# Performance work log

Measured on AMD Instinct MI355X. Metric: run time of the kernel, lower is better.

## Reference

```python
import jax, jax.numpy as jnp
import numpy as np

N_NODES = 100000
N_EDGES = 1600000
D_IN = 128
D_HID = 128
D_OUT = 128


def setup_inputs() -> dict:
    key = jax.random.key(0)
    ks = jax.random.split(key, 6)
    node_features = jax.random.normal(ks[0], (N_NODES, D_IN), dtype=jnp.float32)
    edge_index = jax.random.randint(ks[1], (2, N_EDGES), 0, N_NODES, dtype=jnp.int32)
    s1 = 1.0 / np.sqrt(D_IN)
    s2 = 1.0 / np.sqrt(D_HID)
    W1 = jax.random.normal(ks[2], (D_IN, D_HID), dtype=jnp.float32) * s1
    W2 = jax.random.normal(ks[3], (D_HID, D_HID), dtype=jnp.float32) * s2
    W3 = jax.random.normal(ks[4], (D_HID, D_OUT), dtype=jnp.float32) * s2
    b1 = jnp.zeros((D_HID,), dtype=jnp.float32)
    b2 = jnp.zeros((D_HID,), dtype=jnp.float32)
    b3 = jnp.zeros((D_OUT,), dtype=jnp.float32)
    return {"node_features": node_features, "edge_index": edge_index,
            "W1": W1, "b1": b1, "W2": W2, "b2": b2, "W3": W3, "b3": b3}


def _aggregate(x, src, dst, n_nodes):
    # mean over incoming neighbors (by dst), residual add; degree clamped to >=1
    msg = jax.ops.segment_sum(x[src], dst, num_segments=n_nodes)  # [N, D]
    deg = jax.ops.segment_sum(jnp.ones_like(dst, dtype=x.dtype), dst,
                              num_segments=n_nodes)
    deg = jnp.maximum(deg, 1.0)[:, None]
    return x + msg / deg


def reference(node_features, edge_index, W1, b1, W2, b2, W3, b3):
    n_nodes = node_features.shape[0]
    src, dst = edge_index[0], edge_index[1]
    x = _aggregate(node_features, src, dst, n_nodes)
    x = jax.nn.relu(x @ W1 + b1)
    x = _aggregate(x, src, dst, n_nodes)
    x = jax.nn.relu(x @ W2 + b2)
    x = x.mean(axis=0)  # graph readout -> [D_HID]
    return x @ W3 + b3  # [D_OUT]
```

## Files before the change

### kernel.cpp

```cpp
#include <hip/hip_runtime.h>

#define D 128
#define SLOTS 64
#define NB 391
#define NBANK 4
#define SUBCAP 1536
#define BINCAP (NBANK * SUBCAP)
#define BATCH 2048
#define EPB 8
#define CNTSTRIDE 16
#define WPITCH 136

typedef __attribute__((ext_vector_type(8))) short short8;
typedef __attribute__((ext_vector_type(4))) float float4v;

__device__ inline unsigned short f2bf(float f) {
    union { float f; unsigned u; } a; a.f = f;
    unsigned u = a.u;
    return (unsigned short)((u + 0x7fffu + ((u >> 16) & 1u)) >> 16);
}
__device__ inline unsigned packbf(float a, float b) {
    return (unsigned)f2bf(a) | ((unsigned)f2bf(b) << 16);
}
__device__ inline unsigned pack4fp8(float a, float b, float c, float d) {
    int t = __builtin_amdgcn_cvt_pk_fp8_f32(a, b, 0, false);
    t = __builtin_amdgcn_cvt_pk_fp8_f32(c, d, t, true);
    return (unsigned)t;
}
__device__ inline unsigned char pack1fp8(float a) {
    int t = __builtin_amdgcn_cvt_pk_fp8_f32(a, 0.f, 0, false);
    return (unsigned char)(t & 0xff);
}
__device__ inline void acc8fp8(float* acc, uint2 w) {
    auto f0 = __builtin_amdgcn_cvt_pk_f32_fp8(w.x, false);
    auto f1 = __builtin_amdgcn_cvt_pk_f32_fp8(w.x, true);
    auto f2 = __builtin_amdgcn_cvt_pk_f32_fp8(w.y, false);
    auto f3 = __builtin_amdgcn_cvt_pk_f32_fp8(w.y, true);
    acc[0] += f0[0]; acc[1] += f0[1]; acc[2] += f1[0]; acc[3] += f1[1];
    acc[4] += f2[0]; acc[5] += f2[1]; acc[6] += f3[0]; acc[7] += f3[1];
}


__global__ __launch_bounds__(256) void k_head(const int* __restrict__ src,
                                              const int* __restrict__ dst, int nE,
                                              int* __restrict__ gcnt, int* __restrict__ bins,
                                              const float* __restrict__ x,
                                              unsigned char* __restrict__ y8,
                                              unsigned char* __restrict__ h8dummy,
                                              float* __restrict__ colsum,
                                              int n16, int nBatches) {
    __shared__ int hist[512];
    __shared__ int excl[512];
    __shared__ int base[NB];
    __shared__ int stage[BATCH];
    __shared__ int gofs[BATCH];
    __shared__ int waveSum[4];
    int tid = threadIdx.x;

    if (blockIdx.x >= nBatches) {
        int cb = blockIdx.x - nBatches;
        if (cb == 0) {
            if (tid < 128) colsum[tid] = 0.f;
            else if (tid < 136)
                reinterpret_cast<uint4*>(y8)[(size_t)n16 + (tid - 128)] = make_uint4(0, 0, 0, 0);
            else if (tid < 144)
                reinterpret_cast<uint4*>(h8dummy)[tid - 136] = make_uint4(0, 0, 0, 0);
        }
        int i = cb * 256 + tid;
        if (i < n16) {
            const float4* xin = reinterpret_cast<const float4*>(x) + (size_t)i * 4;
            float4 v0 = xin[0], v1 = xin[1], v2 = xin[2], v3 = xin[3];
            uint4 o;
            o.x = pack4fp8(v0.x, v0.y, v0.z, v0.w);
            o.y = pack4fp8(v1.x, v1.y, v1.z, v1.w);
            o.z = pack4fp8(v2.x, v2.y, v2.z, v2.w);
            o.w = pack4fp8(v3.x, v3.y, v3.z, v3.w);
            reinterpret_cast<uint4*>(y8)[i] = o;
        }
        return;
    }

    int start = blockIdx.x * BATCH;
    int cntB = nE - start; if (cntB > BATCH) cntB = BATCH;
    if (cntB <= 0) return;
    int bank = blockIdx.x & (NBANK - 1);

    hist[tid] = 0; hist[tid + 256] = 0;
    __syncthreads();

    int b[EPB], r[EPB], v[EPB];
    #pragma unroll
    for (int i = 0; i < EPB; ++i) {
        int e = start + i * 256 + tid;
        if (e < nE) {
            int d = dst[e];
            b[i] = d >> 8;
            v[i] = (src[e] << 8) | (d & 255);
            r[i] = atomicAdd(&hist[b[i]], 1);
        } else b[i] = -1;
    }
    __syncthreads();

    int e0 = tid * 2, e1 = e0 + 1;
    int h0 = hist[e0], h1v = hist[e1];
    int s = h0 + h1v;
    int lane = tid & 63, w = tid >> 6;
    int sum = s;
    #pragma unroll
    for (int off2 = 1; off2 < 64; off2 <<= 1) {
        int tmp = __shfl_up(sum, off2, 64);
        if (lane >= off2) sum += tmp;
    }
    if (lane == 63) waveSum[w] = sum;
    __syncthreads();
    int wbase = 0;
    if (w > 0) wbase += waveSum[0];
    if (w > 1) wbase += waveSum[1];
    if (w > 2) wbase += waveSum[2];
    int exclPair = wbase + sum - s;
    excl[e0] = exclPair;
    excl[e1] = exclPair + h0;
    if (tid < NB)
        base[tid] = atomicAdd(&gcnt[(tid * NBANK + bank) * CNTSTRIDE], hist[tid]);
    if (tid + 256 < NB)
        base[tid + 256] = atomicAdd(&gcnt[((tid + 256) * NBANK + bank) * CNTSTRIDE], hist[tid + 256]);
    __syncthreads();

    #pragma unroll
    for (int i = 0; i < EPB; ++i) {
        if (b[i] >= 0) {
            int p = excl[b[i]] + r[i];
            int o = base[b[i]] + r[i];
            stage[p] = v[i];
            gofs[p] = (o < SUBCAP) ? (b[i] * BINCAP + bank * SUBCAP + o) : -1;
        }
    }
    __syncthreads();

    #pragma unroll
    for (int i = 0; i < EPB; ++i) {
        int p = i * 256 + tid;
        if (p < cntB) {
            int g = gofs[p];
            if (g >= 0) bins[g] = stage[p];
        }
    }
}


__global__ __launch_bounds__(256) void k_scatter2(const int* __restrict__ gcnt,
                                                  const int* __restrict__ bins,
                                                  int* __restrict__ slots,
                                                  int* __restrict__ deg, int n, int nAll) {
    __shared__ int slotsL[128 * SLOTS];
    __shared__ int cntL[128];
    __shared__ int cnt4s[128];
    int tid = threadIdx.x;
    int bin = blockIdx.x >> 1;
    int half = blockIdx.x & 1;
    if (tid < 128) cntL[tid] = 0;
    __syncthreads();

    #pragma unroll
    for (int k = 0; k < NBANK; ++k) {
        int c = gcnt[(bin * NBANK + k) * CNTSTRIDE]; if (c > SUBCAP) c = SUBCAP;
        const int* eb = bins + (size_t)bin * BINCAP + k * SUBCAP;
        for (int i = tid; i < c; i += 256) {
            int vv = eb[i];
            int dl = vv & 255;
            if ((dl >> 7) == half) {
                int p = atomicAdd(&cntL[dl & 127], 1);
                if (p < SLOTS) slotsL[(dl & 127) * SLOTS + p] = vv >> 8;
            }
        }
    }
    __syncthreads();

    int node0 = bin * 256 + half * 128;
    int remNodes = n - node0;
    if (remNodes > 128) remNodes = 128;
    if (remNodes < 0) remNodes = 0;

    if (tid < remNodes) {
        int dg = cntL[tid]; if (dg > SLOTS) dg = SLOTS;
        int dgr = (dg + 3) & ~3;
        for (int p = dg; p < dgr; ++p) slotsL[tid * SLOTS + p] = nAll;
        deg[node0 + tid] = dg;
        cnt4s[tid] = dgr;
    }
    __syncthreads();

    uint4* gout = reinterpret_cast<uint4*>(slots + (size_t)node0 * SLOTS);
    const uint4* lin = reinterpret_cast<const uint4*>(slotsL);
    int nv = remNodes * (SLOTS / 4);
    for (int i = tid; i < nv; i += 256) {
        int nd = i >> 4, vec = i & 15;
        if ((vec << 2) < cnt4s[nd]) gout[i] = lin[i];
    }
}


__global__ void k_agg(const unsigned char* __restrict__ Xin8,
                      unsigned short* __restrict__ Xout,
                      const int* __restrict__ deg, const int* __restrict__ slots, int n) {
    int t = blockIdx.x * 256 + threadIdx.x;
    int node = t >> 4;
    int lane = t & 15;
    if (node >= n) return;
    int dg = deg[node];
    int cnt4 = (dg + 3) & ~3;
    float acc[8] = {0.f, 0.f, 0.f, 0.f, 0.f, 0.f, 0.f, 0.f};
    const int* sl = slots + (size_t)node * SLOTS;
    for (int j = 0; j < cnt4; j += 4) {
        int4 s4 = *reinterpret_cast<const int4*>(sl + j);
        uint2 w0 = *reinterpret_cast<const uint2*>(Xin8 + (size_t)s4.x * D + lane * 8);
        uint2 w1 = *reinterpret_cast<const uint2*>(Xin8 + (size_t)s4.y * D + lane * 8);
        uint2 w2 = *reinterpret_cast<const uint2*>(Xin8 + (size_t)s4.z * D + lane * 8);
        uint2 w3 = *reinterpret_cast<const uint2*>(Xin8 + (size_t)s4.w * D + lane * 8);
        acc8fp8(acc, w0); acc8fp8(acc, w1); acc8fp8(acc, w2); acc8fp8(acc, w3);
    }
    float inv = 1.0f / (float)(dg > 0 ? dg : 1);
    uint2 s8 = *reinterpret_cast<const uint2*>(Xin8 + (size_t)node * D + lane * 8);
    float self[8] = {0.f, 0.f, 0.f, 0.f, 0.f, 0.f, 0.f, 0.f};
    acc8fp8(self, s8);
    float o[8];
    #pragma unroll
    for (int k = 0; k < 8; ++k) o[k] = self[k] + acc[k] * inv;
    uint4 ov;
    ov.x = packbf(o[0], o[1]); ov.y = packbf(o[2], o[3]);
    ov.z = packbf(o[4], o[5]); ov.w = packbf(o[6], o[7]);
    reinterpret_cast<uint4*>(Xout + (size_t)node * D)[lane] = ov;
}


__global__ __launch_bounds__(256) void k_gemm(const unsigned short* __restrict__ X,
                                              const float* __restrict__ W,
                                              const float* __restrict__ bias,
                                              unsigned char* __restrict__ Y8,
                                              float* __restrict__ colsum,
                                              int n, int mode) {
    __shared__ unsigned short Wt[128 * WPITCH];
    __shared__ float cs[128];
    int tid = threadIdx.x;
    int wave = tid >> 6, L = tid & 63;
    int m16 = L & 15, g = L >> 4;

    #pragma unroll
    for (int i = 0; i < 8; ++i) {
        int p = i * 256 + tid;
        int col = p & 127, kg = p >> 7;
        unsigned pk[4];
        #pragma unroll
        for (int h = 0; h < 4; ++h) {
            float w0 = W[(kg * 8 + 2 * h + 0) * 128 + col];
            float w1 = W[(kg * 8 + 2 * h + 1) * 128 + col];
            pk[h] = packbf(w0, w1);
        }
        *reinterpret_cast<uint4*>(&Wt[col * WPITCH + kg * 8]) =
            make_uint4(pk[0], pk[1], pk[2], pk[3]);
    }
    if (mode && tid < 128) cs[tid] = 0.f;
    __syncthreads();

    int row0 = blockIdx.x * 128 + wave * 32;
    float4v zero4 = {0.f, 0.f, 0.f, 0.f};
    float4v acc[2][8];
    #pragma unroll
    for (int rt = 0; rt < 2; ++rt)
        #pragma unroll
        for (int ct = 0; ct < 8; ++ct) acc[rt][ct] = zero4;

    #pragma unroll
    for (int q = 0; q < 4; ++q) {
        int k0 = q * 32;
        short8 a[2];
        #pragma unroll
        for (int rt = 0; rt < 2; ++rt) {
            int row = row0 + rt * 16 + m16;
            short8 af = {0, 0, 0, 0, 0, 0, 0, 0};
            if (row < n)
                af = *reinterpret_cast<const short8*>(X + (size_t)row * D + k0 + g * 8);
            a[rt] = af;
        }
        #pragma unroll
        for (int ct = 0; ct < 8; ++ct) {
            short8 b = *reinterpret_cast<const short8*>(&Wt[(ct * 16 + m16) * WPITCH + k0 + g * 8]);
            acc[0][ct] = __builtin_amdgcn_mfma_f32_16x16x32_bf16(a[0], b, acc[0][ct], 0, 0, 0);
            acc[1][ct] = __builtin_amdgcn_mfma_f32_16x16x32_bf16(a[1], b, acc[1][ct], 0, 0, 0);
        }
    }

    float bj[8];
    #pragma unroll
    for (int ct = 0; ct < 8; ++ct) bj[ct] = bias[ct * 16 + m16];

    if (mode == 0) {
        #pragma unroll
        for (int rt = 0; rt < 2; ++rt)
            #pragma unroll
            for (int i = 0; i < 4; ++i) {
                int row = row0 + rt * 16 + g * 4 + i;
                if (row < n) {
                    #pragma unroll
                    for (int ct = 0; ct < 8; ++ct) {
                        float v = fmaxf(acc[rt][ct][i] + bj[ct], 0.f);
                        Y8[(size_t)row * D + ct * 16 + m16] = pack1fp8(v);
                    }
                }
            }
    } else {
        float csv[8] = {0.f, 0.f, 0.f, 0.f, 0.f, 0.f, 0.f, 0.f};
        #pragma unroll
        for (int rt = 0; rt < 2; ++rt)
            #pragma unroll
            for (int i = 0; i < 4; ++i) {
                int row = row0 + rt * 16 + g * 4 + i;
                if (row < n) {
                    #pragma unroll
                    for (int ct = 0; ct < 8; ++ct)
                        csv[ct] += fmaxf(acc[rt][ct][i] + bj[ct], 0.f);
                }
            }
        #pragma unroll
        for (int ct = 0; ct < 8; ++ct) atomicAdd(&cs[ct * 16 + m16], csv[ct]);
        __syncthreads();
        if (tid < 128) atomicAdd(&colsum[tid], cs[tid]);
    }
}


__global__ void k_final(const float* __restrict__ colsum, const float* __restrict__ W3,
                        const float* __restrict__ b3, float* __restrict__ out, float invN) {
    int j = threadIdx.x;
    float acc = b3[j];
    #pragma unroll 8
    for (int k = 0; k < D; ++k)
        acc += colsum[k] * invN * W3[k * D + j];
    out[j] = acc;
}


extern "C" void kernel_launch(void* const* d_in, const int* in_sizes, int n_in,
                              void* d_out, int out_size, void* d_ws, size_t ws_size,
                              hipStream_t stream) {
    const float* nf = (const float*)d_in[0];
    const int*   ei = (const int*)d_in[1];
    const float* W1 = (const float*)d_in[2];
    const float* b1 = (const float*)d_in[3];
    const float* W2 = (const float*)d_in[4];
    const float* b2 = (const float*)d_in[5];
    const float* W3 = (const float*)d_in[6];
    const float* b3 = (const float*)d_in[7];
    float* out = (float*)d_out;

    int n  = in_sizes[0] / D;
    int nE = in_sizes[1] / 2;
    const int* src = ei;
    const int* dst = ei + nE;

    int nBins = (n + 255) / 256;
    int nBatches = (nE + BATCH - 1) / BATCH;
    int n16 = n * (D / 16);

    char* ws = (char*)d_ws;
    size_t off = 0;
    auto alloc = [&](size_t bytes) -> void* {
        off = (off + 255) & ~(size_t)255;
        void* p = ws + off;
        off += bytes;
        return p;
    };
    int* gcnt  = (int*)alloc((size_t)nBins * NBANK * CNTSTRIDE * 4);
    int* bins  = (int*)alloc((size_t)nBins * BINCAP * 4);
    int* slots = (int*)alloc((size_t)nBins * 256 * SLOTS * 4);
    int* deg   = (int*)alloc((size_t)n * 4);
    unsigned char*  x8  = (unsigned char*) alloc((size_t)(n + 1) * D);
    unsigned short* t16 = (unsigned short*)alloc((size_t)n * D * 2);
    unsigned char*  h8  = (unsigned char*) alloc((size_t)(n + 1) * D);
    float* colsum = (float*)alloc(128 * 4);

    hipMemsetAsync(gcnt, 0, (size_t)nBins * NBANK * CNTSTRIDE * 4, stream);

    int gC = (n16 + 255) / 256;
    int gA = (n * 16 + 255) / 256;
    int gG = (n + 127) / 128;

    k_head<<<nBatches + gC, 256, 0, stream>>>(src, dst, nE, gcnt, bins,
                                              nf, x8, h8 + (size_t)n * D,
                                              colsum, n16, nBatches);
    k_scatter2<<<nBins * 2, 256, 0, stream>>>(gcnt, bins, slots, deg, n, n);

    k_agg<<<gA, 256, 0, stream>>>(x8, t16, deg, slots, n);
    k_gemm<<<gG, 256, 0, stream>>>(t16, W1, b1, h8, (float*)nullptr, n, 0);
    k_agg<<<gA, 256, 0, stream>>>(h8, t16, deg, slots, n);
    k_gemm<<<gG, 256, 0, stream>>>(t16, W2, b2, (unsigned char*)nullptr, colsum, n, 1);
    k_final<<<1, 128, 0, stream>>>(colsum, W3, b3, out, 1.0f / (float)n);
}
```

Measured before the change: 257.1 us.

## Fuse final readout into last GEMM block, widen gather unroll, more count banks

```diff
diff --git a/kernel.cpp b/kernel.cpp
--- a/kernel.cpp
+++ b/kernel.cpp
@@ -3,8 +3,8 @@
 #define D 128
 #define SLOTS 64
 #define NB 391
-#define NBANK 4
-#define SUBCAP 1536
+#define NBANK 8
+#define SUBCAP 768
 #define BINCAP (NBANK * SUBCAP)
 #define BATCH 2048
 #define EPB 8
@@ -154,7 +154,7 @@
                                                   int* __restrict__ deg, int n, int nAll) {
     __shared__ int slotsL[128 * SLOTS];
     __shared__ int cntL[128];
-    __shared__ int cnt4s[128];
+    __shared__ int cnt8s[128];
     int tid = threadIdx.x;
     int bin = blockIdx.x >> 1;
     int half = blockIdx.x & 1;
@@ -183,10 +183,10 @@
 
     if (tid < remNodes) {
         int dg = cntL[tid]; if (dg > SLOTS) dg = SLOTS;
-        int dgr = (dg + 3) & ~3;
+        int dgr = (dg + 7) & ~7;
         for (int p = dg; p < dgr; ++p) slotsL[tid * SLOTS + p] = nAll;
         deg[node0 + tid] = dg;
-        cnt4s[tid] = dgr;
+        cnt8s[tid] = dgr;
     }
     __syncthreads();
 
@@ -195,7 +195,7 @@
     int nv = remNodes * (SLOTS / 4);
     for (int i = tid; i < nv; i += 256) {
         int nd = i >> 4, vec = i & 15;
-        if ((vec << 2) < cnt4s[nd]) gout[i] = lin[i];
+        if ((vec << 2) < cnt8s[nd]) gout[i] = lin[i];
     }
 }
 
@@ -208,16 +208,22 @@
     int lane = t & 15;
     if (node >= n) return;
     int dg = deg[node];
-    int cnt4 = (dg + 3) & ~3;
+    int cnt8 = (dg + 7) & ~7;
     float acc[8] = {0.f, 0.f, 0.f, 0.f, 0.f, 0.f, 0.f, 0.f};
     const int* sl = slots + (size_t)node * SLOTS;
-    for (int j = 0; j < cnt4; j += 4) {
-        int4 s4 = *reinterpret_cast<const int4*>(sl + j);
-        uint2 w0 = *reinterpret_cast<const uint2*>(Xin8 + (size_t)s4.x * D + lane * 8);
-        uint2 w1 = *reinterpret_cast<const uint2*>(Xin8 + (size_t)s4.y * D + lane * 8);
-        uint2 w2 = *reinterpret_cast<const uint2*>(Xin8 + (size_t)s4.z * D + lane * 8);
-        uint2 w3 = *reinterpret_cast<const uint2*>(Xin8 + (size_t)s4.w * D + lane * 8);
+    for (int j = 0; j < cnt8; j += 8) {
+        int4 s4a = *reinterpret_cast<const int4*>(sl + j);
+        int4 s4b = *reinterpret_cast<const int4*>(sl + j + 4);
+        uint2 w0 = *reinterpret_cast<const uint2*>(Xin8 + (size_t)s4a.x * D + lane * 8);
+        uint2 w1 = *reinterpret_cast<const uint2*>(Xin8 + (size_t)s4a.y * D + lane * 8);
+        uint2 w2 = *reinterpret_cast<const uint2*>(Xin8 + (size_t)s4a.z * D + lane * 8);
+        uint2 w3 = *reinterpret_cast<const uint2*>(Xin8 + (size_t)s4a.w * D + lane * 8);
+        uint2 w4 = *reinterpret_cast<const uint2*>(Xin8 + (size_t)s4b.x * D + lane * 8);
+        uint2 w5 = *reinterpret_cast<const uint2*>(Xin8 + (size_t)s4b.y * D + lane * 8);
+        uint2 w6 = *reinterpret_cast<const uint2*>(Xin8 + (size_t)s4b.z * D + lane * 8);
+        uint2 w7 = *reinterpret_cast<const uint2*>(Xin8 + (size_t)s4b.w * D + lane * 8);
         acc8fp8(acc, w0); acc8fp8(acc, w1); acc8fp8(acc, w2); acc8fp8(acc, w3);
+        acc8fp8(acc, w4); acc8fp8(acc, w5); acc8fp8(acc, w6); acc8fp8(acc, w7);
     }
     float inv = 1.0f / (float)(dg > 0 ? dg : 1);
     uint2 s8 = *reinterpret_cast<const uint2*>(Xin8 + (size_t)node * D + lane * 8);
@@ -238,9 +244,14 @@
                                               const float* __restrict__ bias,
                                               unsigned char* __restrict__ Y8,
                                               float* __restrict__ colsum,
-                                              int n, int mode) {
+                                              int n, int mode,
+                                              const float* __restrict__ W3,
+                                              const float* __restrict__ b3,
+                                              float* __restrict__ out, float invN,
+                                              int* __restrict__ ticket, int nBlk) {
     __shared__ unsigned short Wt[128 * WPITCH];
     __shared__ float cs[128];
+    __shared__ int isLast;
     int tid = threadIdx.x;
     int wave = tid >> 6, L = tid & 63;
     int m16 = L & 15, g = L >> 4;
@@ -325,18 +336,27 @@
         for (int ct = 0; ct < 8; ++ct) atomicAdd(&cs[ct * 16 + m16], csv[ct]);
         __syncthreads();
         if (tid < 128) atomicAdd(&colsum[tid], cs[tid]);
-    }
-}
-
-
-__global__ void k_final(const float* __restrict__ colsum, const float* __restrict__ W3,
-                        const float* __restrict__ b3, float* __restrict__ out, float invN) {
-    int j = threadIdx.x;
-    float acc = b3[j];
-    #pragma unroll 8
-    for (int k = 0; k < D; ++k)
-        acc += colsum[k] * invN * W3[k * D + j];
-    out[j] = acc;
+        __threadfence();
+        if (tid == 0) {
+            int t = atomicAdd(ticket, 1);
+            isLast = (t == nBlk - 1) ? 1 : 0;
+        }
+        __syncthreads();
+        if (isLast) {
+            __threadfence();
+            if (tid < 128)
+                cs[tid] = __hip_atomic_load(&colsum[tid], __ATOMIC_RELAXED,
+                                            __HIP_MEMORY_SCOPE_AGENT) * invN;
+            __syncthreads();
+            if (tid < 128) {
+                float acc2 = b3[tid];
+                #pragma unroll 8
+                for (int k = 0; k < D; ++k)
+                    acc2 += cs[k] * W3[k * D + tid];
+                out[tid] = acc2;
+            }
+        }
+    }
 }
 
 
@@ -370,7 +390,9 @@
         off += bytes;
         return p;
     };
-    int* gcnt  = (int*)alloc((size_t)nBins * NBANK * CNTSTRIDE * 4);
+    size_t gcntInts = (size_t)nBins * NBANK * CNTSTRIDE;
+    int* gcnt  = (int*)alloc((gcntInts + 16) * 4);
+    int* ticket = gcnt + gcntInts;
     int* bins  = (int*)alloc((size_t)nBins * BINCAP * 4);
     int* slots = (int*)alloc((size_t)nBins * 256 * SLOTS * 4);
     int* deg   = (int*)alloc((size_t)n * 4);
@@ -379,7 +401,7 @@
     unsigned char*  h8  = (unsigned char*) alloc((size_t)(n + 1) * D);
     float* colsum = (float*)alloc(128 * 4);
 
-    hipMemsetAsync(gcnt, 0, (size_t)nBins * NBANK * CNTSTRIDE * 4, stream);
+    hipMemsetAsync(gcnt, 0, (gcntInts + 16) * 4, stream);
 
     int gC = (n16 + 255) / 256;
     int gA = (n * 16 + 255) / 256;
@@ -391,8 +413,10 @@
     k_scatter2<<<nBins * 2, 256, 0, stream>>>(gcnt, bins, slots, deg, n, n);
 
     k_agg<<<gA, 256, 0, stream>>>(x8, t16, deg, slots, n);
-    k_gemm<<<gG, 256, 0, stream>>>(t16, W1, b1, h8, (float*)nullptr, n, 0);
+    k_gemm<<<gG, 256, 0, stream>>>(t16, W1, b1, h8, (float*)nullptr, n, 0,
+                                   (const float*)nullptr, (const float*)nullptr,
+                                   (float*)nullptr, 0.f, (int*)nullptr, 0);
     k_agg<<<gA, 256, 0, stream>>>(h8, t16, deg, slots, n);
-    k_gemm<<<gG, 256, 0, stream>>>(t16, W2, b2, (unsigned char*)nullptr, colsum, n, 1);
-    k_final<<<1, 128, 0, stream>>>(colsum, W3, b3, out, 1.0f / (float)n);
-}
+    k_gemm<<<gG, 256, 0, stream>>>(t16, W2, b2, (unsigned char*)nullptr, colsum, n, 1,
+                                   W3, b3, out, 1.0f / (float)n, ticket, gG);
+}
```

After: 280.4 us. 1.09x slower.
